# Optimization experiments

Hardware: AMD Instinct MI355X
Metric: run time of the kernel (lower is better)

## Reference

```python
import jax, jax.numpy as jnp
import numpy as np

N = 6
DT = 0.02
EPS = 1e-6
_R, _C = np.tril_indices(N)  # row-major lower-triangle order, matches the torch double loop


def _mlp(x, W1, b1, W2, b2, W3, b3):
    h = jax.nn.softplus(x @ W1 + b1)
    h = jax.nn.softplus(h @ W2 + b2)
    return h @ W3 + b3


def _trig(q):
    # interleaved [cos q0, sin q0, cos q1, sin q1, ...]
    return jnp.stack([jnp.cos(q), jnp.sin(q)], axis=-1).reshape(q.shape[:-1] + (2 * N,))


def _mass_single(q, pL):
    # q: (6,) -> M: (6,6)
    y = _mlp(_trig(q), *pL)  # (21,)
    L = jnp.zeros((N, N), y.dtype).at[_R, _C].set(y)
    return L @ L.T + EPS * jnp.eye(N, dtype=y.dtype)


def _mass_batched(q, pL):
    y = _mlp(_trig(q), *pL)  # (B,21)
    L = jnp.zeros((q.shape[0], N, N), y.dtype).at[:, _R, _C].set(y)
    return jnp.einsum('bik,bjk->bij', L, L) + EPS * jnp.eye(N, dtype=y.dtype)


def _pot_batched(q, pV):
    return _mlp(_trig(q), *pV)[:, 0]  # (B,)


def _get_acc(q, qdot, a, pL, pV):
    M = _mass_batched(q, pL)                                   # (B,6,6)
    # per-sample Jacobian dM[i,j]/dq[k] -> (B,6,6,6)
    dM_dq = jax.vmap(jax.jacfwd(lambda qq: _mass_single(qq, pL)))(q)
    # torch: term_1[b,i,j,l] = sum_k M[b,l,k] * dM[b,j,k]/dq[b,i]
    term1 = jnp.einsum('blk,bjki->bijl', M, dM_dq)
    dM = term1 + term1.swapaxes(2, 3)
    c = (jnp.einsum('bjik,bk,bj->bi', dM, qdot, qdot)
         - 0.5 * jnp.einsum('bikj,bk,bj->bi', dM, qdot, qdot))
    # faithful to torch.cholesky_inverse(M): inverse of tril(M) @ tril(M)^T
    Linv = jnp.linalg.inv(jnp.tril(M))
    Minv = Linv.swapaxes(-1, -2) @ Linv
    dV_dq = jax.grad(lambda qq: _pot_batched(qq, pV).sum())(q)  # (B,6)
    return jnp.einsum('bij,bj->bi', Minv, a - c - dV_dq)


def _derivs(s, a, pL, pV):
    q, qdot = s[:, :N], s[:, N:]
    qddot = _get_acc(q, qdot, a, pL, pV)
    return jnp.concatenate([qdot, qddot], axis=1)


def _rk2(s, a, pL, pV):
    alpha = 2.0 / 3.0
    k1 = _derivs(s, a, pL, pV)
    k2 = _derivs(s + alpha * DT * k1, a, pL, pV)
    return s + DT * ((1.0 - 1.0 / (2.0 * alpha)) * k1 + (1.0 / (2.0 * alpha)) * k2)


def setup_inputs() -> dict:
    key = jax.random.key(0)
    ks = jax.random.split(key, 16)
    B = 32768
    def lin(kw, kb, fin, fout):
        s = 1.0 / np.sqrt(fin)
        return (jax.random.uniform(kw, (fin, fout), jnp.float32, -s, s),
                jax.random.uniform(kb, (fout,), jnp.float32, -s, s))
    W1L, b1L = lin(ks[0], ks[1], 12, 128)
    W2L, b2L = lin(ks[2], ks[3], 128, 128)
    W3L, b3L = lin(ks[4], ks[5], 128, 21)
    W1V, b1V = lin(ks[6], ks[7], 12, 128)
    W2V, b2V = lin(ks[8], ks[9], 128, 128)
    W3V, b3V = lin(ks[10], ks[11], 128, 1)
    o = jax.random.normal(ks[12], (B, 18), jnp.float32)
    a = jax.random.normal(ks[13], (B, 6), jnp.float32)
    return {"o": o, "a": a,
            "W1L": W1L, "b1L": b1L, "W2L": W2L, "b2L": b2L, "W3L": W3L, "b3L": b3L,
            "W1V": W1V, "b1V": b1V, "W2V": W2V, "b2V": b2V, "W3V": W3V, "b3V": b3V}


def reference(o, a, W1L, b1L, W2L, b2L, W3L, b3L, W1V, b1V, W2V, b2V, W3V, b3V):
    pL = (W1L, b1L, W2L, b2L, W3L, b3L)
    pV = (W1V, b1V, W2V, b2V, W3V, b3V)
    s = o[:, :2 * N]
    s_next = _rk2(s, a, pL, pV)
    return jnp.concatenate([s_next, o[:, 2 * N:]], axis=1)
```

## Files before the change

kernel.cpp:

```cpp
#include <hip/hip_runtime.h>

#define SMP 64
#define NW 8
#define NT (NW*64)

constexpr float DTc  = 0.02f;
constexpr float ADc  = (2.0f/3.0f)*0.02f;
constexpr float EPSc = 1e-6f;

#define FQ   0
#define FQD  6
#define FT   12
#define FL   24
#define FM   45
#define FDV  81
#define FC1  87
#define FC2  93
#define FKQ  99
#define FGT  105
#define SSTR 117

#define HS 129

__device__ __forceinline__ float softplusf(float z) {
    return fmaxf(z, 0.0f) + __logf(1.0f + __expf(-fabsf(z)));
}
__device__ __forceinline__ float sigmoidf_(float z) {
    float t = __expf(-fabsf(z));
    float r = 1.0f / (1.0f + t);
    return z >= 0.0f ? r : t * r;
}

__global__ void prep_kernel(const float* __restrict__ W1L, const float* __restrict__ W1V,
                            const float* __restrict__ W2V, float* __restrict__ ws) {
    int idx = blockIdx.x*256 + threadIdx.x;
    if (idx < 1536) {
        int n = idx / 12, d = idx % 12;
        ws[idx] = W1L[d*128 + n];
    } else if (idx < 3072) {
        int j = idx - 1536;
        int m = j / 12, d = j % 12;
        ws[idx] = W1V[d*128 + m];
    } else if (idx < 19456) {
        int j = idx - 3072;
        int n = j / 128, m = j % 128;
        ws[idx] = W2V[m*128 + n];
    }
}

__launch_bounds__(NT, 2)
__global__ void lnn_kernel(
    const float* __restrict__ o,   const float* __restrict__ aIn,
    const float* __restrict__ b1L, const float* __restrict__ W2L,
    const float* __restrict__ b2L, const float* __restrict__ W3L,
    const float* __restrict__ b3L,
    const float* __restrict__ b1V, const float* __restrict__ W2V,
    const float* __restrict__ b2V, const float* __restrict__ W3V,
    const float* __restrict__ W1LT, const float* __restrict__ W1VT,
    const float* __restrict__ W2VT,
    float* __restrict__ out)
{
    __shared__ float H1[SMP*HS];
    __shared__ float H2[SMP*HS];
    __shared__ float GH[SMP*HS];
    __shared__ float S[SMP*SSTR];

    const int tid  = threadIdx.x;
    const int lane = tid & 63;
    const int wv   = __builtin_amdgcn_readfirstlane(tid >> 6);
    const int gs   = blockIdx.x * SMP + lane;
    float* Sl = &S[lane*SSTR];
    float* Hrow1 = &H1[lane*HS];
    float* Hrow2 = &H2[lane*HS];
    float* HrowG = &GH[lane*HS];

    constexpr int TRW[21] = {0,1,1,2,2,2,3,3,3,3,4,4,4,4,4,5,5,5,5,5,5};
    constexpr int TCW[21] = {0,0,1,0,1,2,0,1,2,3,0,1,2,3,4,0,1,2,3,4,5};

    for (int stage = 0; stage < 2; ++stage) {
        float qv[6];
        if (stage == 0) {
            #pragma unroll
            for (int i = 0; i < 6; ++i) qv[i] = o[gs*18+i];
            if (wv == 0) {
                #pragma unroll
                for (int i = 0; i < 6; ++i) { Sl[FQ+i] = qv[i]; Sl[FQD+i] = o[gs*18+6+i]; }
            }
        } else {
            #pragma unroll
            for (int i = 0; i < 6; ++i) qv[i] = Sl[FQ+i];
        }
        float tt[12];
        #pragma unroll
        for (int i = 0; i < 6; ++i) { tt[2*i] = cosf(qv[i]); tt[2*i+1] = sinf(qv[i]); }
        if (wv == 0) {
            #pragma unroll
            for (int d = 0; d < 12; ++d) Sl[FT+d] = tt[d];
        } else if (wv == 1) {
            #pragma unroll
            for (int k = 0; k < 21; ++k) Sl[FL+k] = b3L[k];
        } else if (wv == 2) {
            #pragma unroll
            for (int i = 0; i < 6; ++i) { Sl[FC1+i] = 0.0f; Sl[FC2+i] = 0.0f; }
        } else if (wv == 3) {
            #pragma unroll
            for (int d = 0; d < 12; ++d) Sl[FGT+d] = 0.0f;
        }
        {
            const int m0 = __builtin_amdgcn_readfirstlane(wv * 16);
            #pragma unroll
            for (int j = 0; j < 16; ++j) {
                int m = m0 + j;
                const float4* w4 = (const float4*)&W1VT[m*12];
                float4 wa = w4[0], wb = w4[1], wc = w4[2];
                float z = b1V[m];
                z += tt[0]*wa.x + tt[1]*wa.y + tt[2]*wa.z + tt[3]*wa.w;
                z += tt[4]*wb.x + tt[5]*wb.y + tt[6]*wb.z + tt[7]*wb.w;
                z += tt[8]*wc.x + tt[9]*wc.y + tt[10]*wc.z + tt[11]*wc.w;
                Hrow2[m] = softplusf(z);
            }
        }
        __syncthreads();

        {
            const int n0 = __builtin_amdgcn_readfirstlane(wv * 16);
            #pragma unroll
            for (int j = 0; j < 16; ++j) {
                int n = n0 + j;
                const float4* w4 = (const float4*)&W1LT[n*12];
                float4 wa = w4[0], wb = w4[1], wc = w4[2];
                float z = b1L[n];
                z += tt[0]*wa.x + tt[1]*wa.y + tt[2]*wa.z + tt[3]*wa.w;
                z += tt[4]*wb.x + tt[5]*wb.y + tt[6]*wb.z + tt[7]*wb.w;
                z += tt[8]*wc.x + tt[9]*wc.y + tt[10]*wc.z + tt[11]*wc.w;
                Hrow1[n] = softplusf(z);
            }
            float acc[16];
            #pragma unroll
            for (int j = 0; j < 16; ++j) acc[j] = b2V[n0+j];
            for (int m8 = 0; m8 < 128; m8 += 8) {
                float hr[8];
                #pragma unroll
                for (int t = 0; t < 8; ++t) hr[t] = Hrow2[m8+t];
                #pragma unroll
                for (int t = 0; t < 8; ++t) {
                    const float4* w4 = (const float4*)&W2V[(m8+t)*128 + n0];
                    #pragma unroll
                    for (int g = 0; g < 4; ++g) {
                        float4 w = w4[g];
                        acc[4*g+0] += hr[t]*w.x; acc[4*g+1] += hr[t]*w.y;
                        acc[4*g+2] += hr[t]*w.z; acc[4*g+3] += hr[t]*w.w;
                    }
                }
            }
            #pragma unroll
            for (int j = 0; j < 16; ++j) {
                int n = n0 + j;
                HrowG[n] = sigmoidf_(acc[j]) * W3V[n];
            }
        }
        __syncthreads();

        {
            const int n0 = __builtin_amdgcn_readfirstlane(wv * 16);
            float sig1v[16];
            #pragma unroll
            for (int i = 0; i < 16; ++i) sig1v[i] = 1.0f - __expf(-Hrow2[n0+i]);

            float acc[16], ga[16];
            #pragma unroll
            for (int j = 0; j < 16; ++j) { acc[j] = b2L[n0+j]; ga[j] = 0.0f; }
            for (int m8 = 0; m8 < 128; m8 += 8) {
                float hr[8], gr[8];
                #pragma unroll
                for (int t = 0; t < 8; ++t) { hr[t] = Hrow1[m8+t]; gr[t] = HrowG[m8+t]; }
                #pragma unroll
                for (int t = 0; t < 8; ++t) {
                    const float4* w4 = (const float4*)&W2L[(m8+t)*128 + n0];
                    const float4* v4 = (const float4*)&W2VT[(m8+t)*128 + n0];
                    #pragma unroll
                    for (int g = 0; g < 4; ++g) {
                        float4 w = w4[g];
                        acc[4*g+0] += hr[t]*w.x; acc[4*g+1] += hr[t]*w.y;
                        acc[4*g+2] += hr[t]*w.z; acc[4*g+3] += hr[t]*w.w;
                        float4 v = v4[g];
                        ga[4*g+0] += gr[t]*v.x; ga[4*g+1] += gr[t]*v.y;
                        ga[4*g+2] += gr[t]*v.z; ga[4*g+3] += gr[t]*v.w;
                    }
                }
            }
            float yp[21];
            #pragma unroll
            for (int k = 0; k < 21; ++k) yp[k] = 0.0f;
            #pragma unroll
            for (int j = 0; j < 16; ++j) {
                int n = n0 + j;
                float h2 = softplusf(acc[j]);
                Hrow2[n] = h2;
                #pragma unroll
                for (int k = 0; k < 21; ++k) yp[k] += h2 * W3L[n*21 + k];
            }
            #pragma unroll
            for (int k = 0; k < 21; ++k) atomicAdd(&Sl[FL+k], yp[k]);

            float gtp[12];
            #pragma unroll
            for (int d = 0; d < 12; ++d) gtp[d] = 0.0f;
            #pragma unroll
            for (int i = 0; i < 16; ++i) {
                int m = n0 + i;
                float g1h = ga[i] * sig1v[i];
                const float4* w4 = (const float4*)&W1VT[m*12];
                float4 wa = w4[0], wb = w4[1], wc = w4[2];
                gtp[0] += g1h*wa.x; gtp[1] += g1h*wa.y; gtp[2]  += g1h*wa.z; gtp[3]  += g1h*wa.w;
                gtp[4] += g1h*wb.x; gtp[5] += g1h*wb.y; gtp[6]  += g1h*wb.z; gtp[7]  += g1h*wb.w;
                gtp[8] += g1h*wc.x; gtp[9] += g1h*wc.y; gtp[10] += g1h*wc.z; gtp[11] += g1h*wc.w;
            }
            #pragma unroll
            for (int d = 0; d < 12; ++d) atomicAdd(&Sl[FGT+d], gtp[d]);
        }
        __syncthreads();

        if (wv < 6) {
            int i = wv;
            for (int j = 0; j < 6; ++j) {
                float s = 0.0f;
                int mn = (i < j) ? i : j;
                for (int k = 0; k <= mn; ++k)
                    s += Sl[FL + (i*(i+1))/2 + k] * Sl[FL + (j*(j+1))/2 + k];
                if (i == j) s += EPSc;
                Sl[FM + i*6 + j] = s;
            }
        } else if (wv == 6) {
            #pragma unroll
            for (int i = 0; i < 6; ++i)
                Sl[FDV+i] = -tt[2*i+1]*Sl[FGT+2*i] + tt[2*i]*Sl[FGT+2*i+1];
        }
        {
            const int n0 = __builtin_amdgcn_readfirstlane(wv * 16);
            float v1[16], v2[16];
            #pragma unroll
            for (int i = 0; i < 16; ++i) { v1[i] = Hrow1[n0+i]; v2[i] = Hrow2[n0+i]; }
            #pragma unroll
            for (int i = 0; i < 16; ++i) {
                Hrow1[n0+i] = 1.0f - __expf(-v1[i]);
                Hrow2[n0+i] = 1.0f - __expf(-v2[i]);
            }
        }
        __syncthreads();

        {
            float qd[6], u6[6], p6[6], r6[6];
            #pragma unroll
            for (int i = 0; i < 6; ++i) qd[i] = Sl[FQD+i];
            #pragma unroll
            for (int i = 0; i < 6; ++i) {
                float s = 0.0f;
                #pragma unroll
                for (int j = 0; j < 6; ++j) s += Sl[FM+i*6+j]*qd[j];
                u6[i] = s;
            }
            #pragma unroll
            for (int i = 0; i < 6; ++i) { p6[i] = 0.0f; r6[i] = 0.0f; }
            #pragma unroll
            for (int t = 0; t < 21; ++t) {
                float Lv = Sl[FL+t];
                p6[TCW[t]] += Lv * qd[TRW[t]];
                r6[TCW[t]] += Lv * u6[TRW[t]];
            }

            const int n0 = __builtin_amdgcn_readfirstlane(wv * 16);

            float acc[96];
            #pragma unroll
            for (int i = 0; i < 96; ++i) acc[i] = 0.0f;

            for (int m2 = 0; m2 < 128; m2 += 2) {
                float s1a = Hrow1[m2];
                float s1b = Hrow1[m2+1];
                #pragma unroll
                for (int half = 0; half < 2; ++half) {
                    const int mm = m2 + half;
                    const float s1 = half ? s1b : s1a;
                    const float4* w1 = (const float4*)&W1LT[mm*12];
                    float4 wa = w1[0], wb = w1[1], wc = w1[2];
                    float dm[6];
                    dm[0] = s1*(tt[0]*wa.y - tt[1]*wa.x);
                    dm[1] = s1*(tt[2]*wa.w - tt[3]*wa.z);
                    dm[2] = s1*(tt[4]*wb.y - tt[5]*wb.x);
                    dm[3] = s1*(tt[6]*wb.w - tt[7]*wb.z);
                    dm[4] = s1*(tt[8]*wc.y - tt[9]*wc.x);
                    dm[5] = s1*(tt[10]*wc.w - tt[11]*wc.z);
                    const float4* w2 = (const float4*)&W2L[mm*128 + n0];
                    #pragma unroll
                    for (int g = 0; g < 4; ++g) {
                        float4 w = w2[g];
                        #pragma unroll
                        for (int d = 0; d < 6; ++d) {
                            acc[d*16 + 4*g+0] += dm[d]*w.x;
                            acc[d*16 + 4*g+1] += dm[d]*w.y;
                            acc[d*16 + 4*g+2] += dm[d]*w.z;
                            acc[d*16 + 4*g+3] += dm[d]*w.w;
                        }
                    }
                }
            }

            float sig2s[16];
            #pragma unroll
            for (int j = 0; j < 16; ++j) sig2s[j] = Hrow2[n0+j];

            float c1loc[6], c2loc[6];
            #pragma unroll
            for (int i = 0; i < 6; ++i) { c1loc[i] = 0.0f; c2loc[i] = 0.0f; }

            #pragma unroll
            for (int d = 0; d < 6; ++d) {
                float dy[21];
                #pragma unroll
                for (int k = 0; k < 21; ++k) dy[k] = 0.0f;
                #pragma unroll
                for (int j = 0; j < 16; ++j) {
                    float d2 = sig2s[j] * acc[d*16+j];
                    const float* wr = &W3L[(n0+j)*21];
                    #pragma unroll
                    for (int k = 0; k < 21; ++k) dy[k] += d2 * wr[k];
                }
                float a1[6],a2[6],a3[6],a4[6];
                #pragma unroll
                for (int i = 0; i < 6; ++i) { a1[i]=0.f; a2[i]=0.f; a3[i]=0.f; a4[i]=0.f; }
                #pragma unroll
                for (int t = 0; t < 21; ++t) {
                    float dv = dy[t];
                    a1[TRW[t]] += dv * p6[TCW[t]];
                    a2[TCW[t]] += dv * qd[TRW[t]];
                    a3[TRW[t]] += dv * r6[TCW[t]];
                    a4[TCW[t]] += dv * u6[TRW[t]];
                }
                float w6[6], v6[6];
                #pragma unroll
                for (int i = 0; i < 6; ++i) { w6[i] = a1[i]; v6[i] = a3[i]; }
                #pragma unroll
                for (int t = 0; t < 21; ++t) {
                    float Lv = Sl[FL+t];
                    w6[TRW[t]] += Lv * a2[TCW[t]];
                    v6[TRW[t]] += Lv * a4[TCW[t]];
                }
                float qdd = qd[d];
                float uw = 0.0f;
                #pragma unroll
                for (int i = 0; i < 6; ++i) {
                    float mw = 0.0f;
                    #pragma unroll
                    for (int j = 0; j < 6; ++j) mw += Sl[FM+i*6+j]*w6[j];
                    c1loc[i] += qdd*(v6[i]+mw);
                    uw += u6[i]*w6[i];
                }
                c2loc[d] = 2.0f*uw;
            }
            #pragma unroll
            for (int i = 0; i < 6; ++i) atomicAdd(&Sl[FC1+i], c1loc[i]);
            #pragma unroll
            for (int d = 0; d < 6; ++d) atomicAdd(&Sl[FC2+d], c2loc[d]);
        }
        __syncthreads();

        if (wv == 0) {
            float rhs[6];
            #pragma unroll
            for (int i = 0; i < 6; ++i) {
                float c = Sl[FC1+i] - 0.5f*Sl[FC2+i];
                rhs[i] = aIn[gs*6+i] - c - Sl[FDV+i];
            }
            float Mm[36];
            #pragma unroll
            for (int i = 0; i < 36; ++i) Mm[i] = Sl[FM+i];
            float Li[21];
            #pragma unroll
            for (int j = 0; j < 6; ++j) {
                float x[6];
                x[j] = 1.0f / Mm[j*6+j];
                #pragma unroll
                for (int i2 = j+1; i2 < 6; ++i2) {
                    float s = 0.0f;
                    #pragma unroll
                    for (int k = j; k < i2; ++k) s += Mm[i2*6+k]*x[k];
                    x[i2] = -s / Mm[i2*6+i2];
                }
                #pragma unroll
                for (int i2 = j; i2 < 6; ++i2) Li[(i2*(i2+1))/2 + j] = x[i2];
            }
            float y1[6];
            #pragma unroll
            for (int i = 0; i < 6; ++i) {
                float s = 0.0f;
                #pragma unroll
                for (int j = 0; j <= i; ++j) s += Li[(i*(i+1))/2+j]*rhs[j];
                y1[i] = s;
            }
            float qdd2[6];
            #pragma unroll
            for (int i = 0; i < 6; ++i) {
                float s = 0.0f;
                #pragma unroll
                for (int k = i; k < 6; ++k) s += Li[(k*(k+1))/2+i]*y1[k];
                qdd2[i] = s;
            }
            if (stage == 0) {
                #pragma unroll
                for (int i = 0; i < 6; ++i) Sl[FKQ+i] = qdd2[i];
                #pragma unroll
                for (int i = 0; i < 6; ++i) Sl[FQ+i] += ADc*Sl[FQD+i];
                #pragma unroll
                for (int i = 0; i < 6; ++i) Sl[FQD+i] += ADc*qdd2[i];
            } else {
                #pragma unroll
                for (int i = 0; i < 6; ++i) {
                    float q0 = o[gs*18+i], qd0 = o[gs*18+6+i];
                    out[gs*18+i]    = q0  + DTc*(0.25f*qd0      + 0.75f*Sl[FQD+i]);
                    out[gs*18+6+i]  = qd0 + DTc*(0.25f*Sl[FKQ+i] + 0.75f*qdd2[i]);
                    out[gs*18+12+i] = o[gs*18+12+i];
                }
            }
        }
        __syncthreads();
    }
}

extern "C" void kernel_launch(void* const* d_in, const int* in_sizes, int n_in,
                              void* d_out, int out_size, void* d_ws, size_t ws_size,
                              hipStream_t stream) {
    const float* o   = (const float*)d_in[0];
    const float* a   = (const float*)d_in[1];
    const float* W1L = (const float*)d_in[2];
    const float* b1L = (const float*)d_in[3];
    const float* W2L = (const float*)d_in[4];
    const float* b2L = (const float*)d_in[5];
    const float* W3L = (const float*)d_in[6];
    const float* b3L = (const float*)d_in[7];
    const float* W1V = (const float*)d_in[8];
    const float* b1V = (const float*)d_in[9];
    const float* W2V = (const float*)d_in[10];
    const float* b2V = (const float*)d_in[11];
    const float* W3V = (const float*)d_in[12];
    float* ws   = (float*)d_ws;
    float* outp = (float*)d_out;

    hipLaunchKernelGGL(prep_kernel, dim3(76), dim3(256), 0, stream, W1L, W1V, W2V, ws);
    hipLaunchKernelGGL(lnn_kernel, dim3(32768/SMP), dim3(NT), 0, stream,
        o, a, b1L, W2L, b2L, W3L, b3L, b1V, W2V, b2V, W3V,
        ws, ws + 1536, ws + 3072, outp);
}
```

Before: 579.2 us.

## Replace full Jacobian of mass matrix with directional derivatives along qdot

```diff
diff --git a/kernel.cpp b/kernel.cpp
--- a/kernel.cpp
+++ b/kernel.cpp
@@ -1,8 +1,9 @@
 #include <hip/hip_runtime.h>
 
 #define SMP 64
-#define NW 8
+#define NW 16
 #define NT (NW*64)
+#define SLC 8
 
 constexpr float DTc  = 0.02f;
 constexpr float ADc  = (2.0f/3.0f)*0.02f;
@@ -10,15 +11,18 @@
 
 #define FQ   0
 #define FQD  6
-#define FT   12
-#define FL   24
-#define FM   45
-#define FDV  81
-#define FC1  87
-#define FC2  93
-#define FKQ  99
-#define FGT  105
-#define SSTR 117
+#define FL   12
+#define FM   33
+#define FU   69
+#define FP   75
+#define FR   81
+#define FDY  87
+#define FDV  108
+#define FGV  114
+#define FGL  126
+#define FC1  138
+#define FKQ  144
+#define SSTR 151
 
 #define HS 129
 
@@ -30,9 +34,31 @@
     float r = 1.0f / (1.0f + t);
     return z >= 0.0f ? r : t * r;
 }
+__device__ __forceinline__ float dot8(const float4* w, const float* g) {
+    float4 a = w[0], b = w[1];
+    return g[0]*a.x + g[1]*a.y + g[2]*a.z + g[3]*a.w
+         + g[4]*b.x + g[5]*b.y + g[6]*b.z + g[7]*b.w;
+}
+__device__ __forceinline__ void axpy8(float* acc, const float4* w, float h) {
+    float4 a = w[0], b = w[1];
+    acc[0] += h*a.x; acc[1] += h*a.y; acc[2] += h*a.z; acc[3] += h*a.w;
+    acc[4] += h*b.x; acc[5] += h*b.y; acc[6] += h*b.z; acc[7] += h*b.w;
+}
+__device__ __forceinline__ float dot12(const float4* w, const float* v) {
+    float4 a = w[0], b = w[1], c = w[2];
+    return v[0]*a.x + v[1]*a.y + v[2]*a.z + v[3]*a.w
+         + v[4]*b.x + v[5]*b.y + v[6]*b.z + v[7]*b.w
+         + v[8]*c.x + v[9]*c.y + v[10]*c.z + v[11]*c.w;
+}
+__device__ __forceinline__ void axpy12(float* acc, const float4* w, float s) {
+    float4 a = w[0], b = w[1], c = w[2];
+    acc[0] += s*a.x; acc[1] += s*a.y; acc[2]  += s*a.z; acc[3]  += s*a.w;
+    acc[4] += s*b.x; acc[5] += s*b.y; acc[6]  += s*b.z; acc[7]  += s*b.w;
+    acc[8] += s*c.x; acc[9] += s*c.y; acc[10] += s*c.z; acc[11] += s*c.w;
+}
 
 __global__ void prep_kernel(const float* __restrict__ W1L, const float* __restrict__ W1V,
-                            const float* __restrict__ W2V, float* __restrict__ ws) {
+                            float* __restrict__ ws) {
     int idx = blockIdx.x*256 + threadIdx.x;
     if (idx < 1536) {
         int n = idx / 12, d = idx % 12;
@@ -41,14 +67,10 @@
         int j = idx - 1536;
         int m = j / 12, d = j % 12;
         ws[idx] = W1V[d*128 + m];
-    } else if (idx < 19456) {
-        int j = idx - 3072;
-        int n = j / 128, m = j % 128;
-        ws[idx] = W2V[m*128 + n];
     }
 }
 
-__launch_bounds__(NT, 2)
+__launch_bounds__(NT, 4)
 __global__ void lnn_kernel(
     const float* __restrict__ o,   const float* __restrict__ aIn,
     const float* __restrict__ b1L, const float* __restrict__ W2L,
@@ -57,311 +79,285 @@
     const float* __restrict__ b1V, const float* __restrict__ W2V,
     const float* __restrict__ b2V, const float* __restrict__ W3V,
     const float* __restrict__ W1LT, const float* __restrict__ W1VT,
-    const float* __restrict__ W2VT,
     float* __restrict__ out)
 {
     __shared__ float H1[SMP*HS];
-    __shared__ float H2[SMP*HS];
-    __shared__ float GH[SMP*HS];
+    __shared__ float HVs[SMP*HS];
+    __shared__ float G[SMP*HS];
     __shared__ float S[SMP*SSTR];
 
     const int tid  = threadIdx.x;
     const int lane = tid & 63;
     const int wv   = __builtin_amdgcn_readfirstlane(tid >> 6);
     const int gs   = blockIdx.x * SMP + lane;
-    float* Sl = &S[lane*SSTR];
+    const int n0   = __builtin_amdgcn_readfirstlane(wv * SLC);
+    float* Sl    = &S[lane*SSTR];
     float* Hrow1 = &H1[lane*HS];
-    float* Hrow2 = &H2[lane*HS];
-    float* HrowG = &GH[lane*HS];
+    float* HrowV = &HVs[lane*HS];
+    float* HrowG = &G[lane*HS];
 
     constexpr int TRW[21] = {0,1,1,2,2,2,3,3,3,3,4,4,4,4,4,5,5,5,5,5,5};
     constexpr int TCW[21] = {0,0,1,0,1,2,0,1,2,3,0,1,2,3,4,0,1,2,3,4,5};
 
+    float qd[6], tt[12];
+
     for (int stage = 0; stage < 2; ++stage) {
-        float qv[6];
-        if (stage == 0) {
-            #pragma unroll
-            for (int i = 0; i < 6; ++i) qv[i] = o[gs*18+i];
-            if (wv == 0) {
-                #pragma unroll
-                for (int i = 0; i < 6; ++i) { Sl[FQ+i] = qv[i]; Sl[FQD+i] = o[gs*18+6+i]; }
-            }
-        } else {
-            #pragma unroll
-            for (int i = 0; i < 6; ++i) qv[i] = Sl[FQ+i];
-        }
-        float tt[12];
-        #pragma unroll
-        for (int i = 0; i < 6; ++i) { tt[2*i] = cosf(qv[i]); tt[2*i+1] = sinf(qv[i]); }
-        if (wv == 0) {
-            #pragma unroll
-            for (int d = 0; d < 12; ++d) Sl[FT+d] = tt[d];
-        } else if (wv == 1) {
+        {
+            float qv[6];
+            if (stage == 0) {
+                #pragma unroll
+                for (int i = 0; i < 6; ++i) { qv[i] = o[gs*18+i]; qd[i] = o[gs*18+6+i]; }
+                if (wv == 0) {
+                    #pragma unroll
+                    for (int i = 0; i < 6; ++i) { Sl[FQ+i] = qv[i]; Sl[FQD+i] = qd[i]; }
+                }
+            } else {
+                #pragma unroll
+                for (int i = 0; i < 6; ++i) { qv[i] = Sl[FQ+i]; qd[i] = Sl[FQD+i]; }
+            }
+            #pragma unroll
+            for (int i = 0; i < 6; ++i) { tt[2*i] = cosf(qv[i]); tt[2*i+1] = sinf(qv[i]); }
+        }
+        if (wv == 1) {
             #pragma unroll
             for (int k = 0; k < 21; ++k) Sl[FL+k] = b3L[k];
         } else if (wv == 2) {
             #pragma unroll
-            for (int i = 0; i < 6; ++i) { Sl[FC1+i] = 0.0f; Sl[FC2+i] = 0.0f; }
+            for (int k = 0; k < 21; ++k) Sl[FDY+k] = 0.0f;
         } else if (wv == 3) {
             #pragma unroll
-            for (int d = 0; d < 12; ++d) Sl[FGT+d] = 0.0f;
-        }
-        {
-            const int m0 = __builtin_amdgcn_readfirstlane(wv * 16);
-            #pragma unroll
-            for (int j = 0; j < 16; ++j) {
-                int m = m0 + j;
-                const float4* w4 = (const float4*)&W1VT[m*12];
-                float4 wa = w4[0], wb = w4[1], wc = w4[2];
-                float z = b1V[m];
-                z += tt[0]*wa.x + tt[1]*wa.y + tt[2]*wa.z + tt[3]*wa.w;
-                z += tt[4]*wb.x + tt[5]*wb.y + tt[6]*wb.z + tt[7]*wb.w;
-                z += tt[8]*wc.x + tt[9]*wc.y + tt[10]*wc.z + tt[11]*wc.w;
-                Hrow2[m] = softplusf(z);
-            }
-        }
-        __syncthreads();
-
-        {
-            const int n0 = __builtin_amdgcn_readfirstlane(wv * 16);
-            #pragma unroll
-            for (int j = 0; j < 16; ++j) {
+            for (int d = 0; d < 12; ++d) { Sl[FGV+d] = 0.0f; Sl[FGL+d] = 0.0f; }
+        }
+        float h1reg[SLC];
+        #pragma unroll
+        for (int j = 0; j < SLC; ++j) {
+            int m = n0 + j;
+            float zL = b1L[m] + dot12((const float4*)&W1LT[m*12], tt);
+            h1reg[j] = softplusf(zL);
+            Hrow1[m] = h1reg[j];
+            float zV = b1V[m] + dot12((const float4*)&W1VT[m*12], tt);
+            HrowV[m] = softplusf(zV);
+        }
+        __syncthreads();
+
+        float z2reg[SLC];
+        {
+            float accL[SLC], accV[SLC];
+            #pragma unroll
+            for (int j = 0; j < SLC; ++j) { accL[j] = b2L[n0+j]; accV[j] = b2V[n0+j]; }
+            for (int m8 = 0; m8 < 128; m8 += 8) {
+                float h1r[8], hvr[8];
+                #pragma unroll
+                for (int t = 0; t < 8; ++t) { h1r[t] = Hrow1[m8+t]; hvr[t] = HrowV[m8+t]; }
+                #pragma unroll
+                for (int t = 0; t < 8; ++t) {
+                    axpy8(accL, (const float4*)&W2L[(m8+t)*128 + n0], h1r[t]);
+                    axpy8(accV, (const float4*)&W2V[(m8+t)*128 + n0], hvr[t]);
+                }
+            }
+            float yp[21];
+            #pragma unroll
+            for (int k = 0; k < 21; ++k) yp[k] = 0.0f;
+            #pragma unroll
+            for (int j = 0; j < SLC; ++j) {
                 int n = n0 + j;
-                const float4* w4 = (const float4*)&W1LT[n*12];
-                float4 wa = w4[0], wb = w4[1], wc = w4[2];
-                float z = b1L[n];
-                z += tt[0]*wa.x + tt[1]*wa.y + tt[2]*wa.z + tt[3]*wa.w;
-                z += tt[4]*wb.x + tt[5]*wb.y + tt[6]*wb.z + tt[7]*wb.w;
-                z += tt[8]*wc.x + tt[9]*wc.y + tt[10]*wc.z + tt[11]*wc.w;
-                Hrow1[n] = softplusf(z);
-            }
-            float acc[16];
-            #pragma unroll
-            for (int j = 0; j < 16; ++j) acc[j] = b2V[n0+j];
+                HrowG[n] = sigmoidf_(accV[j]) * W3V[n];
+                z2reg[j] = accL[j];
+                float h2 = softplusf(accL[j]);
+                const float* wr = &W3L[n*21];
+                #pragma unroll
+                for (int k = 0; k < 21; ++k) yp[k] += h2 * wr[k];
+            }
+            #pragma unroll
+            for (int k = 0; k < 21; ++k) atomicAdd(&Sl[FL+k], yp[k]);
+        }
+        __syncthreads();
+
+        {
+            float g1v[SLC];
+            #pragma unroll
+            for (int j = 0; j < SLC; ++j) g1v[j] = 0.0f;
+            for (int nn = 0; nn < 128; nn += 8) {
+                float gr[8];
+                #pragma unroll
+                for (int t = 0; t < 8; ++t) gr[t] = HrowG[nn+t];
+                #pragma unroll
+                for (int j = 0; j < SLC; ++j)
+                    g1v[j] += dot8((const float4*)&W2V[(n0+j)*128 + nn], gr);
+            }
+            float gtv[12];
+            #pragma unroll
+            for (int d = 0; d < 12; ++d) gtv[d] = 0.0f;
+            #pragma unroll
+            for (int j = 0; j < SLC; ++j) {
+                float g1h = g1v[j] * (1.0f - __expf(-HrowV[n0+j]));
+                axpy12(gtv, (const float4*)&W1VT[(n0+j)*12], g1h);
+            }
+            #pragma unroll
+            for (int d = 0; d < 12; ++d) atomicAdd(&Sl[FGV+d], gtv[d]);
+        }
+        __syncthreads();
+
+        float s1l[SLC];
+        {
+            float dtv[12];
+            #pragma unroll
+            for (int i = 0; i < 6; ++i) { dtv[2*i] = -tt[2*i+1]*qd[i]; dtv[2*i+1] = tt[2*i]*qd[i]; }
+            #pragma unroll
+            for (int j = 0; j < SLC; ++j) {
+                int m = n0 + j;
+                float dz1 = dot12((const float4*)&W1LT[m*12], dtv);
+                s1l[j] = 1.0f - __expf(-h1reg[j]);
+                HrowV[m] = s1l[j] * dz1;
+            }
+            if (wv == 0) {
+                float Lv[21];
+                #pragma unroll
+                for (int t = 0; t < 21; ++t) Lv[t] = Sl[FL+t];
+                #pragma unroll
+                for (int i = 0; i < 6; ++i) {
+                    #pragma unroll
+                    for (int jj = 0; jj <= i; ++jj) {
+                        float s = 0.0f;
+                        #pragma unroll
+                        for (int k = 0; k <= jj; ++k)
+                            s += Lv[(i*(i+1))/2 + k] * Lv[(jj*(jj+1))/2 + k];
+                        if (i == jj) s += EPSc;
+                        Sl[FM + i*6 + jj] = s;
+                        Sl[FM + jj*6 + i] = s;
+                    }
+                }
+                float um[6];
+                #pragma unroll
+                for (int i = 0; i < 6; ++i) {
+                    float s = 0.0f;
+                    #pragma unroll
+                    for (int jj = 0; jj < 6; ++jj) s += Sl[FM + i*6 + jj] * qd[jj];
+                    um[i] = s; Sl[FU+i] = s;
+                }
+                float pv[6], rv[6];
+                #pragma unroll
+                for (int i = 0; i < 6; ++i) { pv[i] = 0.0f; rv[i] = 0.0f; }
+                #pragma unroll
+                for (int t = 0; t < 21; ++t) {
+                    pv[TCW[t]] += Lv[t] * qd[TRW[t]];
+                    rv[TCW[t]] += Lv[t] * um[TRW[t]];
+                }
+                #pragma unroll
+                for (int i = 0; i < 6; ++i) { Sl[FP+i] = pv[i]; Sl[FR+i] = rv[i]; }
+            } else if (wv == 1) {
+                #pragma unroll
+                for (int i = 0; i < 6; ++i)
+                    Sl[FDV+i] = -tt[2*i+1]*Sl[FGV+2*i] + tt[2*i]*Sl[FGV+2*i+1];
+            }
+        }
+        __syncthreads();
+
+        {
+            float dz2[SLC];
+            #pragma unroll
+            for (int j = 0; j < SLC; ++j) dz2[j] = 0.0f;
             for (int m8 = 0; m8 < 128; m8 += 8) {
-                float hr[8];
-                #pragma unroll
-                for (int t = 0; t < 8; ++t) hr[t] = Hrow2[m8+t];
-                #pragma unroll
-                for (int t = 0; t < 8; ++t) {
-                    const float4* w4 = (const float4*)&W2V[(m8+t)*128 + n0];
-                    #pragma unroll
-                    for (int g = 0; g < 4; ++g) {
-                        float4 w = w4[g];
-                        acc[4*g+0] += hr[t]*w.x; acc[4*g+1] += hr[t]*w.y;
-                        acc[4*g+2] += hr[t]*w.z; acc[4*g+3] += hr[t]*w.w;
+                float dr[8];
+                #pragma unroll
+                for (int t = 0; t < 8; ++t) dr[t] = HrowV[m8+t];
+                #pragma unroll
+                for (int t = 0; t < 8; ++t)
+                    axpy8(dz2, (const float4*)&W2L[(m8+t)*128 + n0], dr[t]);
+            }
+            float sg2[SLC];
+            #pragma unroll
+            for (int j = 0; j < SLC; ++j) sg2[j] = sigmoidf_(z2reg[j]);
+            float dyp[21];
+            #pragma unroll
+            for (int k = 0; k < 21; ++k) dyp[k] = 0.0f;
+            #pragma unroll
+            for (int j = 0; j < SLC; ++j) {
+                float dh2 = sg2[j] * dz2[j];
+                const float* wr = &W3L[(n0+j)*21];
+                #pragma unroll
+                for (int k = 0; k < 21; ++k) dyp[k] += dh2 * wr[k];
+            }
+            #pragma unroll
+            for (int k = 0; k < 21; ++k) atomicAdd(&Sl[FDY+k], dyp[k]);
+            float gy[21];
+            {
+                float uu[6], pp[6], rr[6];
+                #pragma unroll
+                for (int i = 0; i < 6; ++i) { uu[i]=Sl[FU+i]; pp[i]=Sl[FP+i]; rr[i]=Sl[FR+i]; }
+                #pragma unroll
+                for (int t = 0; t < 21; ++t)
+                    gy[t] = uu[TRW[t]]*pp[TCW[t]] + qd[TRW[t]]*rr[TCW[t]];
+            }
+            #pragma unroll
+            for (int j = 0; j < SLC; ++j) {
+                const float* wr = &W3L[(n0+j)*21];
+                float gh2 = 0.0f;
+                #pragma unroll
+                for (int k = 0; k < 21; ++k) gh2 += wr[k] * gy[k];
+                HrowG[n0+j] = sg2[j] * gh2;
+            }
+        }
+        __syncthreads();
+
+        {
+            float gh1[SLC];
+            #pragma unroll
+            for (int j = 0; j < SLC; ++j) gh1[j] = 0.0f;
+            for (int nn = 0; nn < 128; nn += 8) {
+                float gr[8];
+                #pragma unroll
+                for (int t = 0; t < 8; ++t) gr[t] = HrowG[nn+t];
+                #pragma unroll
+                for (int j = 0; j < SLC; ++j)
+                    gh1[j] += dot8((const float4*)&W2L[(n0+j)*128 + nn], gr);
+            }
+            float gtl[12];
+            #pragma unroll
+            for (int d = 0; d < 12; ++d) gtl[d] = 0.0f;
+            #pragma unroll
+            for (int j = 0; j < SLC; ++j) {
+                float gz1 = s1l[j] * gh1[j];
+                axpy12(gtl, (const float4*)&W1LT[(n0+j)*12], gz1);
+            }
+            #pragma unroll
+            for (int d = 0; d < 12; ++d) atomicAdd(&Sl[FGL+d], gtl[d]);
+            if (wv == 1) {
+                float Lv[21], dLv[21];
+                #pragma unroll
+                for (int t = 0; t < 21; ++t) { Lv[t] = Sl[FL+t]; dLv[t] = Sl[FDY+t]; }
+                float B[36];
+                #pragma unroll
+                for (int i = 0; i < 6; ++i) {
+                    #pragma unroll
+                    for (int jj = 0; jj <= i; ++jj) {
+                        float s = 0.0f;
+                        #pragma unroll
+                        for (int k = 0; k <= jj; ++k)
+                            s += dLv[(i*(i+1))/2+k]*Lv[(jj*(jj+1))/2+k]
+                               + Lv[(i*(i+1))/2+k]*dLv[(jj*(jj+1))/2+k];
+                        B[i*6+jj] = s; B[jj*6+i] = s;
                     }
                 }
-            }
-            #pragma unroll
-            for (int j = 0; j < 16; ++j) {
-                int n = n0 + j;
-                HrowG[n] = sigmoidf_(acc[j]) * W3V[n];
-            }
-        }
-        __syncthreads();
-
-        {
-            const int n0 = __builtin_amdgcn_readfirstlane(wv * 16);
-            float sig1v[16];
-            #pragma unroll
-            for (int i = 0; i < 16; ++i) sig1v[i] = 1.0f - __expf(-Hrow2[n0+i]);
-
-            float acc[16], ga[16];
-            #pragma unroll
-            for (int j = 0; j < 16; ++j) { acc[j] = b2L[n0+j]; ga[j] = 0.0f; }
-            for (int m8 = 0; m8 < 128; m8 += 8) {
-                float hr[8], gr[8];
-                #pragma unroll
-                for (int t = 0; t < 8; ++t) { hr[t] = Hrow1[m8+t]; gr[t] = HrowG[m8+t]; }
-                #pragma unroll
-                for (int t = 0; t < 8; ++t) {
-                    const float4* w4 = (const float4*)&W2L[(m8+t)*128 + n0];
-                    const float4* v4 = (const float4*)&W2VT[(m8+t)*128 + n0];
-                    #pragma unroll
-                    for (int g = 0; g < 4; ++g) {
-                        float4 w = w4[g];
-                        acc[4*g+0] += hr[t]*w.x; acc[4*g+1] += hr[t]*w.y;
-                        acc[4*g+2] += hr[t]*w.z; acc[4*g+3] += hr[t]*w.w;
-                        float4 v = v4[g];
-                        ga[4*g+0] += gr[t]*v.x; ga[4*g+1] += gr[t]*v.y;
-                        ga[4*g+2] += gr[t]*v.z; ga[4*g+3] += gr[t]*v.w;
-                    }
-                }
-            }
-            float yp[21];
-            #pragma unroll
-            for (int k = 0; k < 21; ++k) yp[k] = 0.0f;
-            #pragma unroll
-            for (int j = 0; j < 16; ++j) {
-                int n = n0 + j;
-                float h2 = softplusf(acc[j]);
-                Hrow2[n] = h2;
-                #pragma unroll
-                for (int k = 0; k < 21; ++k) yp[k] += h2 * W3L[n*21 + k];
-            }
-            #pragma unroll
-            for (int k = 0; k < 21; ++k) atomicAdd(&Sl[FL+k], yp[k]);
-
-            float gtp[12];
-            #pragma unroll
-            for (int d = 0; d < 12; ++d) gtp[d] = 0.0f;
-            #pragma unroll
-            for (int i = 0; i < 16; ++i) {
-                int m = n0 + i;
-                float g1h = ga[i] * sig1v[i];
-                const float4* w4 = (const float4*)&W1VT[m*12];
-                float4 wa = w4[0], wb = w4[1], wc = w4[2];
-                gtp[0] += g1h*wa.x; gtp[1] += g1h*wa.y; gtp[2]  += g1h*wa.z; gtp[3]  += g1h*wa.w;
-                gtp[4] += g1h*wb.x; gtp[5] += g1h*wb.y; gtp[6]  += g1h*wb.z; gtp[7]  += g1h*wb.w;
-                gtp[8] += g1h*wc.x; gtp[9] += g1h*wc.y; gtp[10] += g1h*wc.z; gtp[11] += g1h*wc.w;
-            }
-            #pragma unroll
-            for (int d = 0; d < 12; ++d) atomicAdd(&Sl[FGT+d], gtp[d]);
-        }
-        __syncthreads();
-
-        if (wv < 6) {
-            int i = wv;
-            for (int j = 0; j < 6; ++j) {
-                float s = 0.0f;
-                int mn = (i < j) ? i : j;
-                for (int k = 0; k <= mn; ++k)
-                    s += Sl[FL + (i*(i+1))/2 + k] * Sl[FL + (j*(j+1))/2 + k];
-                if (i == j) s += EPSc;
-                Sl[FM + i*6 + j] = s;
-            }
-        } else if (wv == 6) {
-            #pragma unroll
-            for (int i = 0; i < 6; ++i)
-                Sl[FDV+i] = -tt[2*i+1]*Sl[FGT+2*i] + tt[2*i]*Sl[FGT+2*i+1];
-        }
-        {
-            const int n0 = __builtin_amdgcn_readfirstlane(wv * 16);
-            float v1[16], v2[16];
-            #pragma unroll
-            for (int i = 0; i < 16; ++i) { v1[i] = Hrow1[n0+i]; v2[i] = Hrow2[n0+i]; }
-            #pragma unroll
-            for (int i = 0; i < 16; ++i) {
-                Hrow1[n0+i] = 1.0f - __expf(-v1[i]);
-                Hrow2[n0+i] = 1.0f - __expf(-v2[i]);
-            }
-        }
-        __syncthreads();
-
-        {
-            float qd[6], u6[6], p6[6], r6[6];
-            #pragma unroll
-            for (int i = 0; i < 6; ++i) qd[i] = Sl[FQD+i];
-            #pragma unroll
-            for (int i = 0; i < 6; ++i) {
-                float s = 0.0f;
-                #pragma unroll
-                for (int j = 0; j < 6; ++j) s += Sl[FM+i*6+j]*qd[j];
-                u6[i] = s;
-            }
-            #pragma unroll
-            for (int i = 0; i < 6; ++i) { p6[i] = 0.0f; r6[i] = 0.0f; }
-            #pragma unroll
-            for (int t = 0; t < 21; ++t) {
-                float Lv = Sl[FL+t];
-                p6[TCW[t]] += Lv * qd[TRW[t]];
-                r6[TCW[t]] += Lv * u6[TRW[t]];
-            }
-
-            const int n0 = __builtin_amdgcn_readfirstlane(wv * 16);
-
-            float acc[96];
-            #pragma unroll
-            for (int i = 0; i < 96; ++i) acc[i] = 0.0f;
-
-            for (int m2 = 0; m2 < 128; m2 += 2) {
-                float s1a = Hrow1[m2];
-                float s1b = Hrow1[m2+1];
-                #pragma unroll
-                for (int half = 0; half < 2; ++half) {
-                    const int mm = m2 + half;
-                    const float s1 = half ? s1b : s1a;
-                    const float4* w1 = (const float4*)&W1LT[mm*12];
-                    float4 wa = w1[0], wb = w1[1], wc = w1[2];
-                    float dm[6];
-                    dm[0] = s1*(tt[0]*wa.y - tt[1]*wa.x);
-                    dm[1] = s1*(tt[2]*wa.w - tt[3]*wa.z);
-                    dm[2] = s1*(tt[4]*wb.y - tt[5]*wb.x);
-                    dm[3] = s1*(tt[6]*wb.w - tt[7]*wb.z);
-                    dm[4] = s1*(tt[8]*wc.y - tt[9]*wc.x);
-                    dm[5] = s1*(tt[10]*wc.w - tt[11]*wc.z);
-                    const float4* w2 = (const float4*)&W2L[mm*128 + n0];
-                    #pragma unroll
-                    for (int g = 0; g < 4; ++g) {
-                        float4 w = w2[g];
-                        #pragma unroll
-                        for (int d = 0; d < 6; ++d) {
-                            acc[d*16 + 4*g+0] += dm[d]*w.x;
-                            acc[d*16 + 4*g+1] += dm[d]*w.y;
-                            acc[d*16 + 4*g+2] += dm[d]*w.z;
-                            acc[d*16 + 4*g+3] += dm[d]*w.w;
-                        }
-                    }
-                }
-            }
-
-            float sig2s[16];
-            #pragma unroll
-            for (int j = 0; j < 16; ++j) sig2s[j] = Hrow2[n0+j];
-
-            float c1loc[6], c2loc[6];
-            #pragma unroll
-            for (int i = 0; i < 6; ++i) { c1loc[i] = 0.0f; c2loc[i] = 0.0f; }
-
-            #pragma unroll
-            for (int d = 0; d < 6; ++d) {
-                float dy[21];
-                #pragma unroll
-                for (int k = 0; k < 21; ++k) dy[k] = 0.0f;
-                #pragma unroll
-                for (int j = 0; j < 16; ++j) {
-                    float d2 = sig2s[j] * acc[d*16+j];
-                    const float* wr = &W3L[(n0+j)*21];
-                    #pragma unroll
-                    for (int k = 0; k < 21; ++k) dy[k] += d2 * wr[k];
-                }
-                float a1[6],a2[6],a3[6],a4[6];
-                #pragma unroll
-                for (int i = 0; i < 6; ++i) { a1[i]=0.f; a2[i]=0.f; a3[i]=0.f; a4[i]=0.f; }
-                #pragma unroll
-                for (int t = 0; t < 21; ++t) {
-                    float dv = dy[t];
-                    a1[TRW[t]] += dv * p6[TCW[t]];
-                    a2[TCW[t]] += dv * qd[TRW[t]];
-                    a3[TRW[t]] += dv * r6[TCW[t]];
-                    a4[TCW[t]] += dv * u6[TRW[t]];
-                }
-                float w6[6], v6[6];
-                #pragma unroll
-                for (int i = 0; i < 6; ++i) { w6[i] = a1[i]; v6[i] = a3[i]; }
-                #pragma unroll
-                for (int t = 0; t < 21; ++t) {
-                    float Lv = Sl[FL+t];
-                    w6[TRW[t]] += Lv * a2[TCW[t]];
-                    v6[TRW[t]] += Lv * a4[TCW[t]];
-                }
-                float qdd = qd[d];
-                float uw = 0.0f;
-                #pragma unroll
-                for (int i = 0; i < 6; ++i) {
-                    float mw = 0.0f;
-                    #pragma unroll
-                    for (int j = 0; j < 6; ++j) mw += Sl[FM+i*6+j]*w6[j];
-                    c1loc[i] += qdd*(v6[i]+mw);
-                    uw += u6[i]*w6[i];
-                }
-                c2loc[d] = 2.0f*uw;
-            }
-            #pragma unroll
-            for (int i = 0; i < 6; ++i) atomicAdd(&Sl[FC1+i], c1loc[i]);
-            #pragma unroll
-            for (int d = 0; d < 6; ++d) atomicAdd(&Sl[FC2+d], c2loc[d]);
+                float uu[6];
+                #pragma unroll
+                for (int i = 0; i < 6; ++i) uu[i] = Sl[FU+i];
+                float Bq[6], Bu[6];
+                #pragma unroll
+                for (int i = 0; i < 6; ++i) {
+                    float s1 = 0.0f, s2 = 0.0f;
+                    #pragma unroll
+                    for (int jj = 0; jj < 6; ++jj) { s1 += B[i*6+jj]*qd[jj]; s2 += B[i*6+jj]*uu[jj]; }
+                    Bq[i] = s1; Bu[i] = s2;
+                }
+                #pragma unroll
+                for (int i = 0; i < 6; ++i) {
+                    float s = 0.0f;
+                    #pragma unroll
+                    for (int jj = 0; jj < 6; ++jj) s += Sl[FM+i*6+jj]*Bq[jj];
+                    Sl[FC1+i] = Bu[i] + s;
+                }
+            }
         }
         __syncthreads();
 
@@ -369,7 +365,8 @@
             float rhs[6];
             #pragma unroll
             for (int i = 0; i < 6; ++i) {
-                float c = Sl[FC1+i] - 0.5f*Sl[FC2+i];
+                float c2i = 2.0f*(-tt[2*i+1]*Sl[FGL+2*i] + tt[2*i]*Sl[FGL+2*i+1]);
+                float c = Sl[FC1+i] - 0.5f*c2i;
                 rhs[i] = aIn[gs*6+i] - c - Sl[FDV+i];
             }
             float Mm[36];
@@ -408,16 +405,16 @@
             }
             if (stage == 0) {
                 #pragma unroll
-                for (int i = 0; i < 6; ++i) Sl[FKQ+i] = qdd2[i];
-                #pragma unroll
-                for (int i = 0; i < 6; ++i) Sl[FQ+i] += ADc*Sl[FQD+i];
-                #pragma unroll
-                for (int i = 0; i < 6; ++i) Sl[FQD+i] += ADc*qdd2[i];
+                for (int i = 0; i < 6; ++i) {
+                    Sl[FKQ+i] = qdd2[i];
+                    Sl[FQ+i]  = Sl[FQ+i] + ADc*qd[i];
+                    Sl[FQD+i] = qd[i] + ADc*qdd2[i];
+                }
             } else {
                 #pragma unroll
                 for (int i = 0; i < 6; ++i) {
                     float q0 = o[gs*18+i], qd0 = o[gs*18+6+i];
-                    out[gs*18+i]    = q0  + DTc*(0.25f*qd0      + 0.75f*Sl[FQD+i]);
+                    out[gs*18+i]    = q0  + DTc*(0.25f*qd0 + 0.75f*qd[i]);
                     out[gs*18+6+i]  = qd0 + DTc*(0.25f*Sl[FKQ+i] + 0.75f*qdd2[i]);
                     out[gs*18+12+i] = o[gs*18+12+i];
                 }
@@ -446,8 +443,8 @@
     float* ws   = (float*)d_ws;
     float* outp = (float*)d_out;
 
-    hipLaunchKernelGGL(prep_kernel, dim3(76), dim3(256), 0, stream, W1L, W1V, W2V, ws);
+    hipLaunchKernelGGL(prep_kernel, dim3(12), dim3(256), 0, stream, W1L, W1V, ws);
     hipLaunchKernelGGL(lnn_kernel, dim3(32768/SMP), dim3(NT), 0, stream,
         o, a, b1L, W2L, b2L, W3L, b3L, b1V, W2V, b2V, W3V,
-        ws, ws + 1536, ws + 3072, outp);
-}
+        ws, ws + 1536, outp);
+}
```

Measured after the change: 675.5 us. +16.6%, slower.
